# Kernel tuning notes

Hardware: AMD Instinct MI355X
Metric: run time of the kernel (lower is better)

## Reference

```python
import jax, jax.numpy as jnp
import numpy as np

N = 50000      # nodes
E = 800000     # edges (avg degree 16)
H = 128        # hidden_dim
F_IN = 128     # node_in_dim
EPS = 1e-8     # torch cosine_similarity eps
ALPHA = 0.3


def _xavier(k, shape):
    fan_out, fan_in = shape
    lim = float(np.sqrt(6.0 / (fan_in + fan_out)))
    return jax.random.uniform(k, shape, minval=-lim, maxval=lim, dtype=jnp.float32)


PARAM_SHAPES = [
    ("w_lq", (H, 1)), ("w_lf", (H, F_IN)),
    ("wq0", (H, 1)), ("wq1", (H, H)), ("wq2", (H, H)),
    ("wx0", (H, F_IN)), ("wx1", (H, H)), ("wx2", (H, H)),
    ("wf0", (H, H)), ("wf1", (H, H)), ("wf2", (H, H)),
    ("m1_w1", (H, H)), ("m1_w2", (H, H)),
    ("m2_w1", (1, H)), ("m2_w2", (1, 1)),
]
BIAS_OF = {"w_lq": "b_lq", "w_lf": "b_lf", "wq0": "bq0", "wq1": "bq1", "wq2": "bq2",
           "wx0": "bx0", "wx1": "bx1", "wx2": "bx2", "wf0": "bf0", "wf1": "bf1",
           "wf2": "bf2", "m1_w1": "m1_b1", "m1_w2": "m1_b2", "m2_w1": "m2_b1", "m2_w2": "m2_b2"}


def setup_inputs() -> dict:
    key = jax.random.key(0)
    ks = jax.random.split(key, 3 + len(PARAM_SHAPES))
    inp = {
        "q": 42,
        "feats": jax.random.normal(ks[0], (N, F_IN), dtype=jnp.float32),
        "edge_index": jax.random.randint(ks[1], (2, E), 0, N, dtype=jnp.int64),
        "neg_edge_index": jax.random.randint(ks[2], (2, E), 0, N, dtype=jnp.int64),
    }
    for i, (name, shape) in enumerate(PARAM_SHAPES):
        inp[name] = _xavier(ks[3 + i], shape)
        inp[BIAS_OF[name]] = jnp.zeros((shape[0],), jnp.float32)
    return inp


def _forward(q, feats, edge_index, neg_edge_index,
             w_lq, b_lq, w_lf, b_lf,
             wq0, bq0, wq1, bq1, wq2, bq2,
             wx0, bx0, wx1, bx1, wx2, bx2,
             wf0, bf0, wf1, bf1, wf2, bf2,
             m1_w1, m1_b1, m1_w2, m1_b2,
             m2_w1, m2_b1, m2_w2, m2_b2):
    n = feats.shape[0]
    src, dst = edge_index[0], edge_index[1]

    # GCN symmetric normalization with self-loops (edge_weight = 1)
    deg = jax.ops.segment_sum(jnp.ones(src.shape[0], feats.dtype), dst, num_segments=n) + 1.0
    dis = deg ** -0.5
    norm_e = dis[src] * dis[dst]        # per-edge norm
    inv_deg = 1.0 / deg                 # self-loop norm d^-1/2 * d^-1/2

    def lin(x, W, b):
        return x @ W.T + b

    def gcn(x, W, b):
        xw = x @ W.T                                                      # [n,H]
        agg = jax.ops.segment_sum(xw[src] * norm_e[:, None], dst, num_segments=n)
        return agg + xw * inv_deg[:, None] + b

    querys = jnp.zeros((n, 1), feats.dtype).at[q, 0].set(1.0)
    querys_ = lin(querys, w_lq, b_lq)
    feats_ = lin(feats, w_lf, b_lf)

    # layer 0
    hq = jax.nn.relu(gcn(querys, wq0, bq0))
    h = jax.nn.relu(gcn(feats, wx0, bx0))
    hf = jax.nn.relu(hq + h + gcn(querys_ + feats_, wf0, bf0))
    # middle layer (num_layers - 2 == 1 iteration, eval mode: dropout identity)
    hq = jax.nn.relu(gcn(hq, wq1, bq1))
    h = jax.nn.relu(gcn(h, wx1, bx1))
    hf = jax.nn.relu(hq + h + gcn(hf, wf1, bf1))
    # final layer (no relu)
    hq = gcn(hq, wq2, bq2)
    h = gcn(h, wx2, bx2)
    hf = hq + h + gcn(hf, wf2, bf2)

    x = lin(jax.nn.relu(lin(hf, m1_w1, m1_b1)), m1_w2, m1_b2)  # mlp1

    # ---- decode (attack_type != 'proposed') ----
    q_emb = x[q]
    qn = jnp.maximum(jnp.linalg.norm(q_emb), EPS)

    def cos_q(v):  # cosine similarity of rows of v with q_emb (torch eps semantics)
        vn = jnp.maximum(jnp.linalg.norm(v, axis=-1), EPS)
        return (v @ q_emb) / (vn * qn)

    # reconstruct loss: BCE-with-logits on cosine edge scores
    pos_s = cos_q((x[src] + x[dst]) * 0.5)
    neg_s = cos_q((x[neg_edge_index[0]] + x[neg_edge_index[1]]) * 0.5)
    loss_recon = jnp.mean(jax.nn.softplus(-pos_s)) + jnp.mean(jax.nn.softplus(neg_s))

    sim_xq = cos_q(x)                                            # [n]
    sim_xx = lin(jax.nn.relu(lin(x, m2_w1, m2_b1)), m2_w2, m2_b2)[:, 0]  # mlp2
    sim = ((1.0 - ALPHA) * sim_xq + ALPHA * sim_xx) * 2.0
    return jax.nn.sigmoid(sim), loss_recon


def reference(q, feats, edge_index, neg_edge_index,
              w_lq, b_lq, w_lf, b_lf,
              wq0, bq0, wq1, bq1, wq2, bq2,
              wx0, bx0, wx1, bx1, wx2, bx2,
              wf0, bf0, wf1, bf1, wf2, bf2,
              m1_w1, m1_b1, m1_w2, m1_b2,
              m2_w1, m2_b1, m2_w2, m2_b2):
    return _forward(q, feats, edge_index, neg_edge_index,
                    w_lq, b_lq, w_lf, b_lf,
                    wq0, bq0, wq1, bq1, wq2, bq2,
                    wx0, bx0, wx1, bx1, wx2, bx2,
                    wf0, bf0, wf1, bf1, wf2, bf2,
                    m1_w1, m1_b1, m1_w2, m1_b2,
                    m2_w1, m2_b1, m2_w2, m2_b2)
```

## Files before the change

### kernel.cpp

```cpp
#include <hip/hip_runtime.h>
#include <math.h>

#define N_NODES 50000
#define N_EDGES 800000
#define EPSV 1e-8f
#define ALPHA 0.3f

typedef __attribute__((ext_vector_type(8))) unsigned short ushort8;
typedef __attribute__((ext_vector_type(4))) float floatx4;
typedef __attribute__((ext_vector_type(2))) long longx2;
typedef _Float16 half8 __attribute__((ext_vector_type(8)));
typedef _Float16 half2v __attribute__((ext_vector_type(2)));

__device__ inline unsigned short f2h(float f) {
    union { _Float16 h; unsigned short u; } c; c.h = (_Float16)f; return c.u;
}
__device__ inline float h2f(unsigned short u) {
    union { unsigned short u; _Float16 h; } c; c.u = u; return (float)c.h;
}
__device__ inline unsigned char f2e4m3(float f) {
    unsigned u = __float_as_uint(f);
    unsigned s = (u >> 24) & 0x80u;
    float af = fabsf(f);
    if (af >= 464.f) return (unsigned char)(s | 0x7Eu);
    if (af < 0.015625f) {
        int m = (int)rintf(af * 512.f);
        return (unsigned char)(s | (unsigned)m);
    }
    unsigned au = __float_as_uint(af);
    unsigned mant = au & 0x7FFFFFu;
    unsigned lsb = (mant >> 20) & 1u;
    mant += 0x7FFFFu + lsb;
    unsigned exp32 = (au >> 23) + (mant >> 23);
    mant &= 0x7FFFFFu;
    unsigned e8 = exp32 - 127u + 7u;
    return (unsigned char)(s | (e8 << 3) | (mant >> 20));
}


__global__ __launch_bounds__(256) void k_count(const int* __restrict__ ei,
                                               int* __restrict__ cnt) {
    int e = blockIdx.x * 256 + threadIdx.x;
    if (e < N_EDGES) atomicAdd(&cnt[ei[N_EDGES + e]], 1);
}

__global__ __launch_bounds__(256) void k_invdis(const int* __restrict__ cnt,
                                                float* __restrict__ dis,
                                                float* __restrict__ inv) {
    int i = blockIdx.x * 256 + threadIdx.x;
    if (i < N_NODES) {
        float d = (float)cnt[i] + 1.0f;
        dis[i] = 1.0f / sqrtf(d);
        inv[i] = 1.0f / d;
    }
}

__global__ __launch_bounds__(256) void k_scan_partial(const int* __restrict__ cnt,
                                                      int* __restrict__ partial) {
    int b = blockIdx.x, t = threadIdx.x;
    int base = b * 1024 + t * 4;
    int s = 0;
#pragma unroll
    for (int j = 0; j < 4; ++j) {
        int idx = base + j;
        if (idx < N_NODES) s += cnt[idx];
    }
// ... 38 lines not shown
    for (int off = 1; off < 256; off <<= 1) {
        int v = 0;
        if (t >= off) v = sh[t - off];
        __syncthreads();
        sh[t] += v;
        __syncthreads();
    }
    int texcl = sh[t] - s;
    int pre = partial[b] + texcl;
#pragma unroll
    for (int j = 0; j < 4; ++j) {
        int idx = base + j;
        if (idx < N_NODES) rowptr[idx] = pre;
        pre += c[j];
    }
}

__global__ __launch_bounds__(256) void k_fill(const int* __restrict__ ei,
                                              const int* __restrict__ rowptr,
                                              int* __restrict__ cursor,
                                              int* __restrict__ col) {
    int e = blockIdx.x * 256 + threadIdx.x;
    if (e < N_EDGES) {
        int d = ei[N_EDGES + e];
        int pos = rowptr[d] + atomicAdd(&cursor[d], 1);
        col[pos] = ei[e];
    }
}

__global__ __launch_bounds__(256) void k_t(const int* __restrict__ ei,
                                           const int* __restrict__ qp,
                                           const float* __restrict__ dis,
                                           const float* __restrict__ inv,
                                           float* __restrict__ t) {
    int e = blockIdx.x * 256 + threadIdx.x;
    int q = *qp;
    if (e == 0) atomicAdd(&t[q], inv[q]);
    if (e < N_EDGES && ei[e] == q) {
        int d = ei[N_EDGES + e];
        atomicAdd(&t[d], dis[q] * dis[d]);
    }
}

__global__ void k_flag(const float* __restrict__ bq0, const float* __restrict__ bq1,
                       int* __restrict__ flag) {
    int j = threadIdx.x;
    float v = (j < 128) ? bq0[j] : bq1[j - 128];
    unsigned long long b = __ballot(v != 0.f);
    __shared__ int bad[4];
    if ((j & 63) == 0) bad[j >> 6] = (b != 0ull);
    __syncthreads();
    if (j == 0) flag[0] = !(bad[0] | bad[1] | bad[2] | bad[3]);
}

__global__ void k_r0(const int* __restrict__ gflag, const float* __restrict__ wq0,
                     float* __restrict__ r0) {
    if (*gflag != 1) return;
    int j = threadIdx.x;
    r0[j] = fmaxf(wq0[j], 0.f);
}

template <int RELU>
__global__ void k_matvec(const int* __restrict__ gflag, const float* __restrict__ W,
                         const float* __restrict__ vin, float* __restrict__ vout) {
    if (*gflag != 1) return;
    int c = blockIdx.x, l = threadIdx.x;
    float2 w = *(const float2*)(W + c * 128 + 2 * l);
    float2 v = *(const float2*)(vin + 2 * l);
    float s = w.x * v.x + w.y * v.y;
#pragma unroll
    for (int m = 1; m < 64; m <<= 1) s += __shfl_xor(s, m, 64);
    if (l == 0) vout[c] = RELU ? fmaxf(s, 0.f) : s;
}

__global__ __launch_bounds__(256) void k_spmv(const int* __restrict__ gflag,
                                              const int* __restrict__ rowptr,
                                              const int* __restrict__ col,
                                              const float* __restrict__ dis,
                                              const float* __restrict__ inv,
                                              const float* __restrict__ vin,
                                              float* __restrict__ vout) {
    if (*gflag != 1) return;
    int i = blockIdx.x * 256 + threadIdx.x;
    if (i >= N_NODES) return;
    int r0 = rowptr[i], r1 = rowptr[i + 1];
    float s = 0.f;
    for (int e = r0; e < r1; ++e) {
        int c = col[e];
        s += dis[c] * vin[c];
    }
    vout[i] = fmaf(inv[i], vin[i], dis[i] * s);
}

__global__ __launch_bounds__(256) void k_cast(const float* __restrict__ in,
                                              unsigned short* __restrict__ out, int n8) {
    int id = blockIdx.x * 256 + threadIdx.x;
    if (id >= n8) return;
    const float4 a = *(const float4*)(in + id * 8);
    const float4 b = *(const float4*)(in + id * 8 + 4);
    ushort8 o;
    o[0] = f2h(a.x); o[1] = f2h(a.y); o[2] = f2h(a.z); o[3] = f2h(a.w);
    o[4] = f2h(b.x); o[5] = f2h(b.y); o[6] = f2h(b.z); o[7] = f2h(b.w);
    *(ushort8*)(out + id * 8) = o;
}

struct WPack { const float* w[11]; };
__global__ __launch_bounds__(256) void k_castw(WPack wp, unsigned short* __restrict__ out) {
    int m = blockIdx.y;
    int id = blockIdx.x * 256 + threadIdx.x;
    const float* src = wp.w[m] + id * 8;
    float4 a = *(const float4*)src;
    float4 b = *(const float4*)(src + 4);
    ushort8 o;
    o[0] = f2h(a.x); o[1] = f2h(a.y); o[2] = f2h(a.z); o[3] = f2h(a.w);
    o[4] = f2h(b.x); o[5] = f2h(b.y); o[6] = f2h(b.z); o[7] = f2h(b.w);
    *(ushort8*)(out + m * 16384 + id * 8) = o;
}

__global__ __launch_bounds__(256) void k_cast8(const float* __restrict__ xf,
                                               unsigned char* __restrict__ xq8) {
    int id = blockIdx.x * 256 + threadIdx.x;
    int node = id >> 3, c = id & 7;
    if (node >= N_NODES) return;
    int kb = c >> 1, mb = (c & 1) * 2;
    const float* base = xf + (size_t)node * 128;
    const float* p0 = base + mb * 32 + kb * 8;
    const float* p1 = base + (mb + 1) * 32 + kb * 8;
    union { unsigned char b[16]; uint4 u; } o;
#pragma unroll
    for (int j = 0; j < 8; ++j) o.b[j] = f2e4m3(p0[j]);
#pragma unroll
    for (int j = 0; j < 8; ++j) o.b[8 + j] = f2e4m3(p1[j]);
    *(uint4*)(xq8 + (size_t)node * 128 + c * 16) = o.u;
}


template <int RELU, int NADD, int HASB2, int WOUT, int RK1>
__global__ __launch_bounds__(256) void k_gemm(
    const unsigned short* __restrict__ A, int As,
    const unsigned short* __restrict__ Wb,
    const float* __restrict__ bias, const float* __restrict__ bias2,
    const unsigned short* __restrict__ add1, int a1s,
    const unsigned short* __restrict__ add2, int a2s,
    const float* __restrict__ u, const float* __restrict__ vq,
    const int* __restrict__ gflag, int want,
    unsigned short* __restrict__ outh, int ohs,
    float* __restrict__ outf, int ofs, int nrows) {
    if (gflag && *gflag != want) return;
    __shared__ unsigned short Al[128 * 128];
    __shared__ unsigned short Wl[128 * 128];
    const int tid = threadIdx.x;
    const int row0 = blockIdx.x * 128;
    const int wv = tid >> 6;
    const int t4 = tid >> 4, c16 = tid & 15;

#pragma unroll
    for (int it = 0; it < 8; ++it) {
        int r = it * 16 + t4;
        int gr = row0 + r; if (gr > nrows - 1) gr = nrows - 1;
        int sw = (c16 * 16) ^ ((r & 7) << 4);
        const char* srcA = (const char*)(A + (size_t)gr * As) + sw;
        __builtin_amdgcn_global_load_lds(
            (const __attribute__((address_space(1))) void*)srcA,
            (__attribute__((address_space(3))) void*)(Al + it * 2048 + wv * 512),
            16, 0, 0);
        const char* srcW = (const char*)(Wb + r * 128) + sw;
        __builtin_amdgcn_global_load_lds(
            (const __attribute__((address_space(1))) void*)srcW,
            (__attribute__((address_space(3))) void*)(Wl + it * 2048 + wv * 512),
            16, 0, 0);
    }
    __syncthreads();

    const int l = tid & 63;
    const int lr = l & 15, lg = l >> 4;
    const int sx = (lr & 7) << 4;

    floatx4 acc[8][2];
#pragma unroll
    for (int i = 0; i < 8; ++i)
#pragma unroll
        for (int j = 0; j < 2; ++j) acc[i][j] = (floatx4){0.f, 0.f, 0.f, 0.f};

#pragma unroll
    for (int ks = 0; ks < 4; ++ks) {
        int ko = (ks * 64 + lg * 16) ^ sx;
        half8 bfr[2];
#pragma unroll
        for (int ct = 0; ct < 2; ++ct) {
            int c = wv * 32 + ct * 16 + lr;
            bfr[ct] = *(const half8*)((char*)Wl + c * 256 + ko);
        }
#pragma unroll
        for (int rt = 0; rt < 8; ++rt) {
            int r = rt * 16 + lr;
            half8 af = *(const half8*)((char*)Al + r * 256 + ko);
            acc[rt][0] = __builtin_amdgcn_mfma_f32_16x16x32_f16(af, bfr[0], acc[rt][0], 0, 0, 0);
            acc[rt][1] = __builtin_amdgcn_mfma_f32_16x16x32_f16(af, bfr[1], acc[rt][1], 0, 0, 0);
        }
    }

#pragma unroll
    for (int ct = 0; ct < 2; ++ct) {
        int colc = wv * 32 + ct * 16 + lr;
        float bv = bias[colc];
        if (HASB2) bv += bias2[colc];
        float vqc = RK1 ? vq[colc] : 0.f;
#pragma unroll
        for (int rt = 0; rt < 8; ++rt) {
            int rbase = row0 + rt * 16 + lg * 4;
#pragma unroll
            for (int reg = 0; reg < 4; ++reg) {
                int r = rbase + reg;
                if (r >= nrows) continue;
                float v = acc[rt][ct][reg] + bv;
                if (RK1) v = fmaf(u[r], vqc, v);
                if (NADD >= 1) v += h2f(add1[(size_t)r * a1s + colc]);
                if (NADD >= 2) v += h2f(add2[(size_t)r * a2s + colc]);
                if (RELU) v = fmaxf(v, 0.f);
                if (WOUT) outf[(size_t)r * ofs + colc] = v;
                else outh[(size_t)r * ohs + colc] = f2h(v);
            }
        }
    }
}


template <int NUM>
__global__ __launch_bounds__(256) void k_agg(
    const int* __restrict__ gflag, int want,
    const int* __restrict__ rowptr, const int* __restrict__ col,
    const float* __restrict__ dis, const float* __restrict__ inv,
    const unsigned short* __restrict__ in0, int s0,
    const unsigned short* __restrict__ in1, int s1,
    const unsigned short* __restrict__ in2, int s2,
    unsigned short* __restrict__ out, int o0, int o1, int o2) {
    if (gflag && *gflag != want) return;
    int i = blockIdx.x * 4 + (threadIdx.x >> 6);
    int l = threadIdx.x & 63;
    int g = l >> 4, li = l & 15;
    int r0 = rowptr[i], r1 = rowptr[i + 1];

    half2v accA[NUM][4], accB[NUM][4];
#pragma unroll
    for (int b = 0; b < NUM; ++b)
#pragma unroll
        for (int j = 0; j < 4; ++j) {
            accA[b][j] = (half2v){(_Float16)0, (_Float16)0};
            accB[b][j] = (half2v){(_Float16)0, (_Float16)0};
        }

    union U8 { ushort8 u; half2v h[4]; };
    const unsigned short* ins[3] = {in0, in1, in2};
    const int ss[3] = {s0, s1, s2};

    for (int base = r0; base < r1; base += 8) {
        int eA = base + g, eB = base + 4 + g;
        int sA = i; float wA = 0.f;
        if (eA < r1) { sA = col[eA]; wA = dis[sA]; }
        int sB = i; float wB = 0.f;
// ... 23 lines not shown
            c.h = accA[b][j] + accB[b][j];
            o.i = __shfl_xor(c.i, 16, 64); c.h += o.h;
            o.i = __shfl_xor(c.i, 32, 64); c.h += o.h;
            accA[b][j] = c.h;
        }
    if (g == 0) {
        float di = dis[i], iv = inv[i];
        const int oo[3] = {o0, o1, o2};
#pragma unroll
        for (int b = 0; b < NUM; ++b) {
            U8 sv;
            sv.u = *(const ushort8*)(ins[b] + (size_t)i * ss[b] + li * 8);
            ushort8 o;
#pragma unroll
            for (int j = 0; j < 4; ++j) {
                float a0 = fmaf(di, (float)accA[b][j][0], iv * (float)sv.h[j][0]);
                float a1 = fmaf(di, (float)accA[b][j][1], iv * (float)sv.h[j][1]);
                o[2 * j] = f2h(a0);
                o[2 * j + 1] = f2h(a1);
            }
            *(ushort8*)(out + (size_t)i * 384 + oo[b] + li * 8) = o;
        }
    }
}

__global__ __launch_bounds__(256) void k_hq0(const int* __restrict__ gflag,
                                             const float* __restrict__ t,
                                             const float* __restrict__ wq0,
                                             const float* __restrict__ bq0,
                                             unsigned short* __restrict__ B1h) {
    if (*gflag != 0) return;
    int gidx = blockIdx.x * 256 + threadIdx.x;
    int i = gidx >> 7, j = gidx & 127;
    B1h[(size_t)i * 384 + j] = f2h(fmaxf(fmaf(t[i], wq0[j], bq0[j]), 0.f));
}

__global__ void k_addwlq(const int* __restrict__ qp, const float* __restrict__ w_lq,
                         unsigned short* __restrict__ z0h) {
    int j = threadIdx.x;
    int q = *qp;
    z0h[(size_t)q * 128 + j] = f2h(h2f(z0h[(size_t)q * 128 + j]) + w_lq[j]);
}


__global__ void k_qemb(const int* __restrict__ qp, const float* __restrict__ xf,
                       float* __restrict__ qe) {
// ... 41 lines not shown
        float s2 = fmaxf(l1, 0.f) * m2w2[0] + m2b2[0];
        float sim = ((1.f - ALPHA) * simq + ALPHA * s2) * 2.f;
        out[node] = 1.f / (1.f + expf(-sim));
        a[node] = dq;
        n2[node] = dx;
    }
}

__global__ __launch_bounds__(256) void k_loss(const int* __restrict__ ei,
                                              const int* __restrict__ nei,
                                              const unsigned char* __restrict__ xq8,
                                              const float* __restrict__ a,
                                              const float* __restrict__ n2,
                                              const float* __restrict__ qe,
                                              float* __restrict__ lossout) {
    int l = threadIdx.x & 63, wvi = threadIdx.x >> 6;
    int i16 = l & 15;
    int kb = l >> 4;
    int gw = blockIdx.x * 4 + wvi;
    const int NW = gridDim.x * 4;
    const int NT = 2 * N_EDGES / 16;
    float qn = qe[128];
    float local = 0.f;

    int t = gw;
    for (; t + NW < NT; t += 2 * NW) {
        int baseA = t * 16;
        int negA = baseA >= N_EDGES;
        const int* EpA = negA ? nei : ei;
        int eoA = negA ? baseA - N_EDGES : baseA;
        int sA = EpA[eoA + i16], dA = EpA[eoA + i16 + N_EDGES];

        int baseB = (t + NW) * 16;
        int negB = baseB >= N_EDGES;
        const int* EpB = negB ? nei : ei;
        int eoB = negB ? baseB - N_EDGES : baseB;
        int sB = EpB[eoB + i16], dB = EpB[eoB + i16 + N_EDGES];

        const unsigned char* psA = xq8 + (size_t)sA * 128 + kb * 32;
        const unsigned char* pdA = xq8 + (size_t)dA * 128 + kb * 32;
        longx2 a01A = *(const longx2*)psA;
        longx2 a23A = *(const longx2*)(psA + 16);
        longx2 b01A = *(const longx2*)pdA;
        longx2 b23A = *(const longx2*)(pdA + 16);

        const unsigned char* psB = xq8 + (size_t)sB * 128 + kb * 32;
        const unsigned char* pdB = xq8 + (size_t)dB * 128 + kb * 32;
        longx2 a01B = *(const longx2*)psB;
        longx2 a23B = *(const longx2*)(psB + 16);
        longx2 b01B = *(const longx2*)pdB;
        longx2 b23B = *(const longx2*)(pdB + 16);

        float n2sA = 0.f, n2dA = 0.f, asA = 0.f, adA = 0.f;
        float n2sB = 0.f, n2dB = 0.f, asB = 0.f, adB = 0.f;
        if (l < 16) {
            n2sA = n2[sA]; n2dA = n2[dA]; asA = a[sA]; adA = a[dA];
            n2sB = n2[sB]; n2dB = n2[dB]; asB = a[sB]; adB = a[dB];
        }

        int r = l & 3;
        int srcl = ((i16 >> 2) << 4) + i16;
        {
            floatx4 acc = (floatx4){0.f, 0.f, 0.f, 0.f};
            acc = __builtin_amdgcn_mfma_f32_16x16x32_fp8_fp8(a01A[0], b01A[0], acc, 0, 0, 0);
            acc = __builtin_amdgcn_mfma_f32_16x16x32_fp8_fp8(a01A[1], b01A[1], acc, 0, 0, 0);
            acc = __builtin_amdgcn_mfma_f32_16x16x32_fp8_fp8(a23A[0], b23A[0], acc, 0, 0, 0);
            acc = __builtin_amdgcn_mfma_f32_16x16x32_fp8_fp8(a23A[1], b23A[1], acc, 0, 0, 0);
            float v = acc[0];
            v = (r == 1) ? acc[1] : v;
            v = (r == 2) ? acc[2] : v;
            v = (r == 3) ? acc[3] : v;
            float dsd = __int_as_float(
                __builtin_amdgcn_ds_bpermute(srcl << 2, __float_as_int(v)));
            if (l < 16) {
                float nv = 0.25f * (n2sA + n2dA + 2.f * dsd);
                float vn = fmaxf(sqrtf(fmaxf(nv, 0.f)), EPSV);
                float cs = (0.5f * (asA + adA)) / (vn * qn);
                float sg = negA ? cs : -cs;
                local += log1pf(expf(sg));
            }
        }
        {
            floatx4 acc = (floatx4){0.f, 0.f, 0.f, 0.f};
            acc = __builtin_amdgcn_mfma_f32_16x16x32_fp8_fp8(a01B[0], b01B[0], acc, 0, 0, 0);
            acc = __builtin_amdgcn_mfma_f32_16x16x32_fp8_fp8(a01B[1], b01B[1], acc, 0, 0, 0);
            acc = __builtin_amdgcn_mfma_f32_16x16x32_fp8_fp8(a23B[0], b23B[0], acc, 0, 0, 0);
            acc = __builtin_amdgcn_mfma_f32_16x16x32_fp8_fp8(a23B[1], b23B[1], acc, 0, 0, 0);
            float v = acc[0];
            v = (r == 1) ? acc[1] : v;
            v = (r == 2) ? acc[2] : v;
            v = (r == 3) ? acc[3] : v;
            float dsd = __int_as_float(
                __builtin_amdgcn_ds_bpermute(srcl << 2, __float_as_int(v)));
            if (l < 16) {
                float nv = 0.25f * (n2sB + n2dB + 2.f * dsd);
                float vn = fmaxf(sqrtf(fmaxf(nv, 0.f)), EPSV);
                float cs = (0.5f * (asB + adB)) / (vn * qn);
                float sg = negB ? cs : -cs;
                local += log1pf(expf(sg));
            }
        }
    }
    if (t < NT) {
        int base = t * 16;
        int neg = base >= N_EDGES;
        const int* Ep = neg ? nei : ei;
        int eo = neg ? base - N_EDGES : base;
        int s = Ep[eo + i16], d = Ep[eo + i16 + N_EDGES];
        const unsigned char* ps = xq8 + (size_t)s * 128 + kb * 32;
        const unsigned char* pd = xq8 + (size_t)d * 128 + kb * 32;
        longx2 a01 = *(const longx2*)ps;
        longx2 a23 = *(const longx2*)(ps + 16);
        longx2 b01 = *(const longx2*)pd;
        longx2 b23 = *(const longx2*)(pd + 16);
        floatx4 acc = (floatx4){0.f, 0.f, 0.f, 0.f};
        acc = __builtin_amdgcn_mfma_f32_16x16x32_fp8_fp8(a01[0], b01[0], acc, 0, 0, 0);
        acc = __builtin_amdgcn_mfma_f32_16x16x32_fp8_fp8(a01[1], b01[1], acc, 0, 0, 0);
        acc = __builtin_amdgcn_mfma_f32_16x16x32_fp8_fp8(a23[0], b23[0], acc, 0, 0, 0);
        acc = __builtin_amdgcn_mfma_f32_16x16x32_fp8_fp8(a23[1], b23[1], acc, 0, 0, 0);
        int r = l & 3;
        float v = acc[0];
        v = (r == 1) ? acc[1] : v;
        v = (r == 2) ? acc[2] : v;
        v = (r == 3) ? acc[3] : v;
        int srcl = ((i16 >> 2) << 4) + i16;
        float dsd = __int_as_float(
            __builtin_amdgcn_ds_bpermute(srcl << 2, __float_as_int(v)));
        if (l < 16) {
            float nv = 0.25f * (n2[s] + n2[d] + 2.f * dsd);
            float vn = fmaxf(sqrtf(fmaxf(nv, 0.f)), EPSV);
            float cs = (0.5f * (a[s] + a[d])) / (vn * qn);
            float sg = neg ? cs : -cs;
            local += log1pf(expf(sg));
        }
    }
    local += __shfl_xor(local, 1, 64);
    local += __shfl_xor(local, 2, 64);
    local += __shfl_xor(local, 4, 64);
    local += __shfl_xor(local, 8, 64);
    __shared__ float sh[4];
    if (l == 0) sh[wvi] = local;
    __syncthreads();
    if (threadIdx.x == 0)
        atomicAdd(lossout, (sh[0] + sh[1] + sh[2] + sh[3]) * (1.f / N_EDGES));
}


extern "C" void kernel_launch(void* const* d_in, const int* in_sizes, int n_in,
// ... 48 lines not shown
    unsigned short* z0h = (unsigned short*)alloc((size_t)N_NODES * 128 * 2);
    unsigned short* B1h = (unsigned short*)alloc((size_t)N_NODES * 384 * 2);
    unsigned short* B2h = (unsigned short*)alloc((size_t)N_NODES * 384 * 2);
    unsigned char* xq8 = (unsigned char*)alloc((size_t)N_NODES * 128);
    float* xf = (float*)alloc((size_t)N_NODES * 128 * 4);

    const int EB = (N_EDGES + 255) / 256;
    const int NB = (N_NODES + 255) / 256;
    const int NP = (N_NODES + 1023) / 1024;
    const int GB = (N_NODES + 127) / 128;

    hipMemsetAsync(cnt, 0, N_NODES * 4, stream);
    hipMemsetAsync(cursor, 0, N_NODES * 4, stream);
    hipMemsetAsync(t, 0, N_NODES * 4, stream);
    hipMemsetAsync(out + N_NODES, 0, 4, stream);

    k_count<<<EB, 256, 0, stream>>>(ei, cnt);
    k_invdis<<<NB, 256, 0, stream>>>(cnt, dis, inv);
    k_scan_partial<<<NP, 256, 0, stream>>>(cnt, partial);
    k_scan_mid<<<1, 64, 0, stream>>>(partial, rowptr);
    k_scan_final<<<NP, 256, 0, stream>>>(cnt, partial, rowptr);
    k_fill<<<EB, 256, 0, stream>>>(ei, rowptr, cursor, col);
    k_t<<<EB, 256, 0, stream>>>(ei, qp, dis, inv, t);
    k_flag<<<1, 256, 0, stream>>>(bq0, bq1, flag);
    k_cast<<<(N_NODES * 128 / 8 + 255) / 256, 256, 0, stream>>>(feats, featsh,
                                                                N_NODES * 128 / 8);
    WPack wp{{w_lf, wx0, wf0, wq1, wx1, wf1, wq2, wx2, wf2, m1w1, m1w2}};
    k_castw<<<dim3(8, 11), 256, 0, stream>>>(wp, Wb);

    k_r0<<<1, 128, 0, stream>>>(flag, wq0, r0v);
    k_spmv<<<NB, 256, 0, stream>>>(flag, rowptr, col, dis, inv, t, u1);
    k_spmv<<<NB, 256, 0, stream>>>(flag, rowptr, col, dis, inv, u1, u2);
    k_matvec<1><<<128, 64, 0, stream>>>(flag, wq1, r0v, r1v);
    k_matvec<0><<<128, 64, 0, stream>>>(flag, wq2, r1v, g2v);

    k_gemm<0, 0, 1, 0, 0><<<GB, 256, 0, stream>>>(featsh, 128, Wb + 0 * 16384, b_lf, b_lq,
                                                  nullptr, 0, nullptr, 0,
                                                  nullptr, nullptr, nullptr, 0,
                                                  z0h, 128, nullptr, 0, N_NODES);
    k_addwlq<<<1, 128, 0, stream>>>(qp, w_lq, z0h);

    k_hq0<<<(N_NODES * 128) / 256, 256, 0, stream>>>(flag, t, wq0, bq0, B1h);
    k_agg<2><<<N_NODES / 4, 256, 0, stream>>>(nullptr, 0, rowptr, col, dis, inv,
                                              featsh, 128, z0h, 128, nullptr, 0,
                                              B2h, 128, 256, 0);
    k_gemm<1, 0, 0, 0, 0><<<GB, 256, 0, stream>>>(B2h + 128, 384, Wb + 1 * 16384, bx0, nullptr,
                                                  nullptr, 0, nullptr, 0,
                                                  nullptr, nullptr, nullptr, 0,
                                                  B1h + 128, 384, nullptr, 0, N_NODES);
    k_gemm<1, 2, 0, 0, 0><<<GB, 256, 0, stream>>>(B2h + 256, 384, Wb + 2 * 16384, bf0, nullptr,
                                                  B1h + 0, 384, B1h + 128, 384,
                                                  nullptr, nullptr, flag, 0,
                                                  B1h + 256, 384, nullptr, 0, N_NODES);
    k_gemm<1, 1, 0, 0, 1><<<GB, 256, 0, stream>>>(B2h + 256, 384, Wb + 2 * 16384, bf0, nullptr,
                                                  B1h + 128, 384, nullptr, 0,
                                                  t, r0v, flag, 1,
                                                  B1h + 256, 384, nullptr, 0, N_NODES);

    k_agg<3><<<N_NODES / 4, 256, 0, stream>>>(flag, 0, rowptr, col, dis, inv,
                                              B1h, 384, B1h + 128, 384, B1h + 256, 384,
                                              B2h, 0, 128, 256);
    k_agg<2><<<N_NODES / 4, 256, 0, stream>>>(flag, 1, rowptr, col, dis, inv,
                                              B1h + 128, 384, B1h + 256, 384, nullptr, 0,
                                              B2h, 128, 256, 0);
    k_gemm<1, 0, 0, 0, 0><<<GB, 256, 0, stream>>>(B2h + 0, 384, Wb + 3 * 16384, bq1, nullptr,
                                                  nullptr, 0, nullptr, 0,
                                                  nullptr, nullptr, flag, 0,
                                                  B1h + 0, 384, nullptr, 0, N_NODES);
    k_gemm<1, 0, 0, 0, 0><<<GB, 256, 0, stream>>>(B2h + 128, 384, Wb + 4 * 16384, bx1, nullptr,
                                                  nullptr, 0, nullptr, 0,
                                                  nullptr, nullptr, nullptr, 0,
                                                  B1h + 128, 384, nullptr, 0, N_NODES);
    k_gemm<1, 2, 0, 0, 0><<<GB, 256, 0, stream>>>(B2h + 256, 384, Wb + 5 * 16384, bf1, nullptr,
                                                  B1h + 0, 384, B1h + 128, 384,
                                                  nullptr, nullptr, flag, 0,
                                                  B1h + 256, 384, nullptr, 0, N_NODES);
    k_gemm<1, 1, 0, 0, 1><<<GB, 256, 0, stream>>>(B2h + 256, 384, Wb + 5 * 16384, bf1, nullptr,
                                                  B1h + 128, 384, nullptr, 0,
                                                  u1, r1v, flag, 1,
                                                  B1h + 256, 384, nullptr, 0, N_NODES);

    k_agg<3><<<N_NODES / 4, 256, 0, stream>>>(flag, 0, rowptr, col, dis, inv,
                                              B1h, 384, B1h + 128, 384, B1h + 256, 384,
                                              B2h, 0, 128, 256);
    k_agg<2><<<N_NODES / 4, 256, 0, stream>>>(flag, 1, rowptr, col, dis, inv,
                                              B1h + 128, 384, B1h + 256, 384, nullptr, 0,
                                              B2h, 128, 256, 0);
    k_gemm<0, 0, 0, 0, 0><<<GB, 256, 0, stream>>>(B2h + 0, 384, Wb + 6 * 16384, bq2, nullptr,
                                                  nullptr, 0, nullptr, 0,
                                                  nullptr, nullptr, flag, 0,
                                                  B1h + 0, 384, nullptr, 0, N_NODES);
    k_gemm<0, 0, 0, 0, 0><<<GB, 256, 0, stream>>>(B2h + 128, 384, Wb + 7 * 16384, bx2, nullptr,
                                                  nullptr, 0, nullptr, 0,
                                                  nullptr, nullptr, nullptr, 0,
                                                  B1h + 128, 384, nullptr, 0, N_NODES);
    k_gemm<0, 2, 0, 0, 0><<<GB, 256, 0, stream>>>(B2h + 256, 384, Wb + 8 * 16384, bf2, nullptr,
                                                  B1h + 0, 384, B1h + 128, 384,
                                                  nullptr, nullptr, flag, 0,
                                                  B1h + 256, 384, nullptr, 0, N_NODES);
    k_gemm<0, 1, 1, 0, 1><<<GB, 256, 0, stream>>>(B2h + 256, 384, Wb + 8 * 16384, bf2, bq2,
                                                  B1h + 128, 384, nullptr, 0,
                                                  u2, g2v, flag, 1,
                                                  B1h + 256, 384, nullptr, 0, N_NODES);

    k_gemm<1, 0, 0, 0, 0><<<GB, 256, 0, stream>>>(B1h + 256, 384, Wb + 9 * 16384, m1b1, nullptr,
                                                  nullptr, 0, nullptr, 0,
                                                  nullptr, nullptr, nullptr, 0,
                                                  B2h + 0, 384, nullptr, 0, N_NODES);
    k_gemm<0, 0, 0, 1, 0><<<GB, 256, 0, stream>>>(B2h + 0, 384, Wb + 10 * 16384, m1b2, nullptr,
                                                  nullptr, 0, nullptr, 0,
                                                  nullptr, nullptr, nullptr, 0,
                                                  nullptr, 0, xf, 128, N_NODES);

    k_cast8<<<(N_NODES * 8 + 255) / 256, 256, 0, stream>>>(xf, xq8);
    k_qemb<<<1, 128, 0, stream>>>(qp, xf, qe);
    k_node<<<N_NODES / 4, 256, 0, stream>>>(xf, qe, m2w1, m2b1, m2w2, m2b2, out, a, n2);
    k_loss<<<2048, 256, 0, stream>>>(ei, nei, xq8, a, n2, qe, out + N_NODES);
}
```

Before: 612.2 us.

## Merge flag-gated kernel pairs, fuse fp8 cast into final GEMM, deepen loss pipelining

Several kernels that were launched in pairs and early-exited on a runtime flag are merged into single kernels that branch on the flag inside: aggregation, the fused-layer GEMM, and the rank-1 setup matvecs. The fp8 quantisation of the output embedding now happens in the last GEMM's epilogue, which removes the separate cast kernel and one re-read of the fp32 output. The loss kernel now keeps four edge batches in flight instead of two, and edge-index loads use nontemporal hints. Together these are meant to cut launch count and redundant memory traffic, at the cost of more registers in the loss loop and scattered byte stores in the GEMM epilogue.

```diff
diff --git a/kernel.cpp b/kernel.cpp
--- a/kernel.cpp
+++ b/kernel.cpp
@@ -36,12 +36,15 @@
     unsigned e8 = exp32 - 127u + 7u;
     return (unsigned char)(s | (e8 << 3) | (mant >> 20));
 }
+__device__ inline int qperm(int k) {
+    return ((k >> 3) & 3) * 32 + (k >> 5) * 8 + (k & 7);
+}
 
 
 __global__ __launch_bounds__(256) void k_count(const int* __restrict__ ei,
                                                int* __restrict__ cnt) {
     int e = blockIdx.x * 256 + threadIdx.x;
-    if (e < N_EDGES) atomicAdd(&cnt[ei[N_EDGES + e]], 1);
+    if (e < N_EDGES) atomicAdd(&cnt[__builtin_nontemporal_load(ei + N_EDGES + e)], 1);
 }
 
 __global__ __launch_bounds__(256) void k_invdis(const int* __restrict__ cnt,
@@ -126,9 +129,9 @@
                                               int* __restrict__ col) {
     int e = blockIdx.x * 256 + threadIdx.x;
     if (e < N_EDGES) {
-        int d = ei[N_EDGES + e];
+        int d = __builtin_nontemporal_load(ei + N_EDGES + e);
         int pos = rowptr[d] + atomicAdd(&cursor[d], 1);
-        col[pos] = ei[e];
+        col[pos] = __builtin_nontemporal_load(ei + e);
     }
 }
 
@@ -140,41 +143,45 @@
     int e = blockIdx.x * 256 + threadIdx.x;
     int q = *qp;
     if (e == 0) atomicAdd(&t[q], inv[q]);
-    if (e < N_EDGES && ei[e] == q) {
+    if (e < N_EDGES && __builtin_nontemporal_load(ei + e) == q) {
         int d = ei[N_EDGES + e];
         atomicAdd(&t[d], dis[q] * dis[d]);
     }
 }
 
-__global__ void k_flag(const float* __restrict__ bq0, const float* __restrict__ bq1,
-                       int* __restrict__ flag) {
+__global__ void k_rank1(const float* __restrict__ bq0, const float* __restrict__ bq1,
+                        const float* __restrict__ wq0, const float* __restrict__ wq1,
+                        const float* __restrict__ wq2, int* __restrict__ flag,
+                        float* __restrict__ r0v, float* __restrict__ r1v,
+                        float* __restrict__ g2v) {
     int j = threadIdx.x;
-    float v = (j < 128) ? bq0[j] : bq1[j - 128];
-    unsigned long long b = __ballot(v != 0.f);
-    __shared__ int bad[4];
+    unsigned long long b = __ballot(bq0[j] != 0.f || bq1[j] != 0.f);
+    __shared__ int bad[2];
+    __shared__ float r0s[128], r1s[128];
     if ((j & 63) == 0) bad[j >> 6] = (b != 0ull);
     __syncthreads();
-    if (j == 0) flag[0] = !(bad[0] | bad[1] | bad[2] | bad[3]);
-}
-
-__global__ void k_r0(const int* __restrict__ gflag, const float* __restrict__ wq0,
-                     float* __restrict__ r0) {
-    if (*gflag != 1) return;
-    int j = threadIdx.x;
-    r0[j] = fmaxf(wq0[j], 0.f);
-}
-
-template <int RELU>
-__global__ void k_matvec(const int* __restrict__ gflag, const float* __restrict__ W,
-                         const float* __restrict__ vin, float* __restrict__ vout) {
-    if (*gflag != 1) return;
-    int c = blockIdx.x, l = threadIdx.x;
-    float2 w = *(const float2*)(W + c * 128 + 2 * l);
-    float2 v = *(const float2*)(vin + 2 * l);
-    float s = w.x * v.x + w.y * v.y;
-#pragma unroll
-    for (int m = 1; m < 64; m <<= 1) s += __shfl_xor(s, m, 64);
-    if (l == 0) vout[c] = RELU ? fmaxf(s, 0.f) : s;
+    int fl = !(bad[0] | bad[1]);
+    if (j == 0) flag[0] = fl;
+    if (!fl) return;
+    float r0 = fmaxf(wq0[j], 0.f);
+    r0s[j] = r0;
+    r0v[j] = r0;
+    __syncthreads();
+    float s = 0.f;
+    for (int k = 0; k < 128; k += 4) {
+        float4 w = *(const float4*)(wq1 + j * 128 + k);
+        s += w.x * r0s[k] + w.y * r0s[k + 1] + w.z * r0s[k + 2] + w.w * r0s[k + 3];
+    }
+    float r1 = fmaxf(s, 0.f);
+    r1s[j] = r1;
+    r1v[j] = r1;
+    __syncthreads();
+    float s2 = 0.f;
+    for (int k = 0; k < 128; k += 4) {
+        float4 w = *(const float4*)(wq2 + j * 128 + k);
+        s2 += w.x * r1s[k] + w.y * r1s[k + 1] + w.z * r1s[k + 2] + w.w * r1s[k + 3];
+    }
+    g2v[j] = s2;
 }
 
 __global__ __launch_bounds__(256) void k_spmv(const int* __restrict__ gflag,
@@ -221,40 +228,12 @@
     *(ushort8*)(out + m * 16384 + id * 8) = o;
 }
 
-__global__ __launch_bounds__(256) void k_cast8(const float* __restrict__ xf,
-                                               unsigned char* __restrict__ xq8) {
-    int id = blockIdx.x * 256 + threadIdx.x;
-    int node = id >> 3, c = id & 7;
-    if (node >= N_NODES) return;
-    int kb = c >> 1, mb = (c & 1) * 2;
-    const float* base = xf + (size_t)node * 128;
-    const float* p0 = base + mb * 32 + kb * 8;
-    const float* p1 = base + (mb + 1) * 32 + kb * 8;
-    union { unsigned char b[16]; uint4 u; } o;
-#pragma unroll
-    for (int j = 0; j < 8; ++j) o.b[j] = f2e4m3(p0[j]);
-#pragma unroll
-    for (int j = 0; j < 8; ++j) o.b[8 + j] = f2e4m3(p1[j]);
-    *(uint4*)(xq8 + (size_t)node * 128 + c * 16) = o.u;
-}
-
-
-template <int RELU, int NADD, int HASB2, int WOUT, int RK1>
-__global__ __launch_bounds__(256) void k_gemm(
+
+__device__ __forceinline__ void gemm_core(
     const unsigned short* __restrict__ A, int As,
-    const unsigned short* __restrict__ Wb,
-    const float* __restrict__ bias, const float* __restrict__ bias2,
-    const unsigned short* __restrict__ add1, int a1s,
-    const unsigned short* __restrict__ add2, int a2s,
-    const float* __restrict__ u, const float* __restrict__ vq,
-    const int* __restrict__ gflag, int want,
-    unsigned short* __restrict__ outh, int ohs,
-    float* __restrict__ outf, int ofs, int nrows) {
-    if (gflag && *gflag != want) return;
-    __shared__ unsigned short Al[128 * 128];
-    __shared__ unsigned short Wl[128 * 128];
+    const unsigned short* __restrict__ Wb, int nrows, int row0,
+    unsigned short* Al, unsigned short* Wl, floatx4 (&acc)[8][2]) {
     const int tid = threadIdx.x;
-    const int row0 = blockIdx.x * 128;
     const int wv = tid >> 6;
     const int t4 = tid >> 4, c16 = tid & 15;
 
@@ -280,7 +259,6 @@
     const int lr = l & 15, lg = l >> 4;
     const int sx = (lr & 7) << 4;
 
-    floatx4 acc[8][2];
 #pragma unroll
     for (int i = 0; i < 8; ++i)
 #pragma unroll
@@ -303,13 +281,31 @@
             acc[rt][1] = __builtin_amdgcn_mfma_f32_16x16x32_f16(af, bfr[1], acc[rt][1], 0, 0, 0);
         }
     }
-
+}
+
+template <int RELU, int HASB2, int WOUT>
+__global__ __launch_bounds__(256) void k_gemm(
+    const unsigned short* __restrict__ A, int As,
+    const unsigned short* __restrict__ Wb,
+    const float* __restrict__ bias, const float* __restrict__ bias2,
+    const int* __restrict__ gflag, int want,
+    unsigned short* __restrict__ outh, int ohs,
+    float* __restrict__ outf, unsigned char* __restrict__ outq, int nrows) {
+    if (gflag && *gflag != want) return;
+    __shared__ unsigned short Al[128 * 128];
+    __shared__ unsigned short Wl[128 * 128];
+    const int row0 = blockIdx.x * 128;
+    floatx4 acc[8][2];
+    gemm_core(A, As, Wb, nrows, row0, Al, Wl, acc);
+
+    const int l = threadIdx.x & 63, wv = threadIdx.x >> 6;
+    const int lr = l & 15, lg = l >> 4;
 #pragma unroll
     for (int ct = 0; ct < 2; ++ct) {
         int colc = wv * 32 + ct * 16 + lr;
         float bv = bias[colc];
         if (HASB2) bv += bias2[colc];
-        float vqc = RK1 ? vq[colc] : 0.f;
+        int qp_ = WOUT == 2 ? qperm(colc) : 0;
 #pragma unroll
         for (int rt = 0; rt < 8; ++rt) {
             int rbase = row0 + rt * 16 + lg * 4;
@@ -318,28 +314,73 @@
                 int r = rbase + reg;
                 if (r >= nrows) continue;
                 float v = acc[rt][ct][reg] + bv;
-                if (RK1) v = fmaf(u[r], vqc, v);
-                if (NADD >= 1) v += h2f(add1[(size_t)r * a1s + colc]);
-                if (NADD >= 2) v += h2f(add2[(size_t)r * a2s + colc]);
                 if (RELU) v = fmaxf(v, 0.f);
-                if (WOUT) outf[(size_t)r * ofs + colc] = v;
-                else outh[(size_t)r * ohs + colc] = f2h(v);
+                if (WOUT == 2) {
+                    outf[(size_t)r * 128 + colc] = v;
+                    outq[(size_t)r * 128 + qp_] = f2e4m3(v);
+                } else {
+                    outh[(size_t)r * ohs + colc] = f2h(v);
+                }
             }
         }
     }
 }
 
+template <int RELU>
+__global__ __launch_bounds__(256) void k_gemmF(
+    const unsigned short* __restrict__ A, int As,
+    const unsigned short* __restrict__ Wb,
+    const float* __restrict__ bias, const float* __restrict__ bias2,
+    const unsigned short* __restrict__ addh, int ahs,
+    const unsigned short* __restrict__ addhq, int aqs,
+    const float* __restrict__ u, const float* __restrict__ vq,
+    const int* __restrict__ gflag,
+    unsigned short* __restrict__ outh, int ohs, int nrows) {
+    __shared__ unsigned short Al[128 * 128];
+    __shared__ unsigned short Wl[128 * 128];
+    const int row0 = blockIdx.x * 128;
+    floatx4 acc[8][2];
+    gemm_core(A, As, Wb, nrows, row0, Al, Wl, acc);
+
+    const int fl = *gflag;
+    const int l = threadIdx.x & 63, wv = threadIdx.x >> 6;
+    const int lr = l & 15, lg = l >> 4;
+#pragma unroll
+    for (int ct = 0; ct < 2; ++ct) {
+        int colc = wv * 32 + ct * 16 + lr;
+        float bv = bias[colc];
+        float vqc = 0.f;
+        if (fl) {
+            vqc = vq[colc];
+            if (bias2) bv += bias2[colc];
+        }
+#pragma unroll
+        for (int rt = 0; rt < 8; ++rt) {
+            int rbase = row0 + rt * 16 + lg * 4;
+#pragma unroll
+            for (int reg = 0; reg < 4; ++reg) {
+                int r = rbase + reg;
+                if (r >= nrows) continue;
+                float v = acc[rt][ct][reg] + bv;
+                if (fl) v = fmaf(u[r], vqc, v);
+                else v += h2f(addhq[(size_t)r * aqs + colc]);
+                v += h2f(addh[(size_t)r * ahs + colc]);
+                if (RELU) v = fmaxf(v, 0.f);
+                outh[(size_t)r * ohs + colc] = f2h(v);
+            }
+        }
+    }
+}
+
 
 template <int NUM>
-__global__ __launch_bounds__(256) void k_agg(
-    const int* __restrict__ gflag, int want,
+__device__ __forceinline__ void agg_body(
     const int* __restrict__ rowptr, const int* __restrict__ col,
     const float* __restrict__ dis, const float* __restrict__ inv,
     const unsigned short* __restrict__ in0, int s0,
     const unsigned short* __restrict__ in1, int s1,
     const unsigned short* __restrict__ in2, int s2,
     unsigned short* __restrict__ out, int o0, int o1, int o2) {
-    if (gflag && *gflag != want) return;
     int i = blockIdx.x * 4 + (threadIdx.x >> 6);
     int l = threadIdx.x & 63;
     int g = l >> 4, li = l & 15;
@@ -409,6 +450,28 @@
             *(ushort8*)(out + (size_t)i * 384 + oo[b] + li * 8) = o;
         }
     }
+}
+
+__global__ __launch_bounds__(256) void k_agg0(
+    const int* __restrict__ rowptr, const int* __restrict__ col,
+    const float* __restrict__ dis, const float* __restrict__ inv,
+    const unsigned short* __restrict__ featsh, const unsigned short* __restrict__ z0h,
+    unsigned short* __restrict__ out) {
+    agg_body<2>(rowptr, col, dis, inv, featsh, 128, z0h, 128, nullptr, 0,
+                out, 128, 256, 0);
+}
+
+__global__ __launch_bounds__(256) void k_aggL(
+    const int* __restrict__ gflag,
+    const int* __restrict__ rowptr, const int* __restrict__ col,
+    const float* __restrict__ dis, const float* __restrict__ inv,
+    const unsigned short* __restrict__ B1h, unsigned short* __restrict__ B2h) {
+    if (*gflag == 1)
+        agg_body<2>(rowptr, col, dis, inv, B1h + 128, 384, B1h + 256, 384,
+                    nullptr, 0, B2h, 128, 256, 0);
+    else
+        agg_body<3>(rowptr, col, dis, inv, B1h, 384, B1h + 128, 384,
+                    B1h + 256, 384, B2h, 0, 128, 256);
 }
 
 __global__ __launch_bounds__(256) void k_hq0(const int* __restrict__ gflag,
@@ -496,86 +559,60 @@
     const int NT = 2 * N_EDGES / 16;
     float qn = qe[128];
     float local = 0.f;
+    const int rsel = l & 3;
+    const int srcl = ((i16 >> 2) << 4) + i16;
 
     int t = gw;
-    for (; t + NW < NT; t += 2 * NW) {
-        int baseA = t * 16;
-        int negA = baseA >= N_EDGES;
-        const int* EpA = negA ? nei : ei;
-        int eoA = negA ? baseA - N_EDGES : baseA;
-        int sA = EpA[eoA + i16], dA = EpA[eoA + i16 + N_EDGES];
-
-        int baseB = (t + NW) * 16;
-        int negB = baseB >= N_EDGES;
-        const int* EpB = negB ? nei : ei;
-        int eoB = negB ? baseB - N_EDGES : baseB;
-        int sB = EpB[eoB + i16], dB = EpB[eoB + i16 + N_EDGES];
-
-        const unsigned char* psA = xq8 + (size_t)sA * 128 + kb * 32;
-        const unsigned char* pdA = xq8 + (size_t)dA * 128 + kb * 32;
-        longx2 a01A = *(const longx2*)psA;
-        longx2 a23A = *(const longx2*)(psA + 16);
-        longx2 b01A = *(const longx2*)pdA;
-        longx2 b23A = *(const longx2*)(pdA + 16);
-
-        const unsigned char* psB = xq8 + (size_t)sB * 128 + kb * 32;
-        const unsigned char* pdB = xq8 + (size_t)dB * 128 + kb * 32;
-        longx2 a01B = *(const longx2*)psB;
-        longx2 a23B = *(const longx2*)(psB + 16);
-        longx2 b01B = *(const longx2*)pdB;
-        longx2 b23B = *(const longx2*)(pdB + 16);
-
-        float n2sA = 0.f, n2dA = 0.f, asA = 0.f, adA = 0.f;
-        float n2sB = 0.f, n2dB = 0.f, asB = 0.f, adB = 0.f;
-        if (l < 16) {
-            n2sA = n2[sA]; n2dA = n2[dA]; asA = a[sA]; adA = a[dA];
-            n2sB = n2[sB]; n2dB = n2[dB]; asB = a[sB]; adB = a[dB];
-        }
-
-        int r = l & 3;
-        int srcl = ((i16 >> 2) << 4) + i16;
-        {
+    for (; t + 3 * NW < NT; t += 4 * NW) {
+        int s[4], d[4], neg[4];
+        longx2 a01[4], a23[4], b01[4], b23[4];
+        float n2s[4], n2d[4], as_[4], ad_[4];
+#pragma unroll
+        for (int p_ = 0; p_ < 4; ++p_) {
+            int base = (t + p_ * NW) * 16;
+            neg[p_] = base >= N_EDGES;
+            const int* Ep = neg[p_] ? nei : ei;
+            int eo = neg[p_] ? base - N_EDGES : base;
+            s[p_] = __builtin_nontemporal_load(Ep + eo + i16);
+            d[p_] = __builtin_nontemporal_load(Ep + eo + i16 + N_EDGES);
+        }
+#pragma unroll
+        for (int p_ = 0; p_ < 4; ++p_) {
+            const unsigned char* ps = xq8 + (size_t)s[p_] * 128 + kb * 32;
+            const unsigned char* pd = xq8 + (size_t)d[p_] * 128 + kb * 32;
+            a01[p_] = *(const longx2*)ps;
+            a23[p_] = *(const longx2*)(ps + 16);
+            b01[p_] = *(const longx2*)pd;
+            b23[p_] = *(const longx2*)(pd + 16);
+            n2s[p_] = 0.f; n2d[p_] = 0.f; as_[p_] = 0.f; ad_[p_] = 0.f;
+            if (l < 16) {
+                n2s[p_] = n2[s[p_]]; n2d[p_] = n2[d[p_]];
+                as_[p_] = a[s[p_]]; ad_[p_] = a[d[p_]];
+            }
+        }
+#pragma unroll
+        for (int p_ = 0; p_ < 4; ++p_) {
             floatx4 acc = (floatx4){0.f, 0.f, 0.f, 0.f};
-            acc = __builtin_amdgcn_mfma_f32_16x16x32_fp8_fp8(a01A[0], b01A[0], acc, 0, 0, 0);
-            acc = __builtin_amdgcn_mfma_f32_16x16x32_fp8_fp8(a01A[1], b01A[1], acc, 0, 0, 0);
-            acc = __builtin_amdgcn_mfma_f32_16x16x32_fp8_fp8(a23A[0], b23A[0], acc, 0, 0, 0);
-            acc = __builtin_amdgcn_mfma_f32_16x16x32_fp8_fp8(a23A[1], b23A[1], acc, 0, 0, 0);
+            acc = __builtin_amdgcn_mfma_f32_16x16x32_fp8_fp8(a01[p_][0], b01[p_][0], acc, 0, 0, 0);
+            acc = __builtin_amdgcn_mfma_f32_16x16x32_fp8_fp8(a01[p_][1], b01[p_][1], acc, 0, 0, 0);
+            acc = __builtin_amdgcn_mfma_f32_16x16x32_fp8_fp8(a23[p_][0], b23[p_][0], acc, 0, 0, 0);
+            acc = __builtin_amdgcn_mfma_f32_16x16x32_fp8_fp8(a23[p_][1], b23[p_][1], acc, 0, 0, 0);
             float v = acc[0];
-            v = (r == 1) ? acc[1] : v;
-            v = (r == 2) ? acc[2] : v;
-            v = (r == 3) ? acc[3] : v;
+            v = (rsel == 1) ? acc[1] : v;
+            v = (rsel == 2) ? acc[2] : v;
+            v = (rsel == 3) ? acc[3] : v;
             float dsd = __int_as_float(
                 __builtin_amdgcn_ds_bpermute(srcl << 2, __float_as_int(v)));
             if (l < 16) {
-                float nv = 0.25f * (n2sA + n2dA + 2.f * dsd);
+                float nv = 0.25f * (n2s[p_] + n2d[p_] + 2.f * dsd);
                 float vn = fmaxf(sqrtf(fmaxf(nv, 0.f)), EPSV);
-                float cs = (0.5f * (asA + adA)) / (vn * qn);
-                float sg = negA ? cs : -cs;
+                float cs = (0.5f * (as_[p_] + ad_[p_])) / (vn * qn);
+                float sg = neg[p_] ? cs : -cs;
                 local += log1pf(expf(sg));
             }
         }
-        {
-            floatx4 acc = (floatx4){0.f, 0.f, 0.f, 0.f};
-            acc = __builtin_amdgcn_mfma_f32_16x16x32_fp8_fp8(a01B[0], b01B[0], acc, 0, 0, 0);
-            acc = __builtin_amdgcn_mfma_f32_16x16x32_fp8_fp8(a01B[1], b01B[1], acc, 0, 0, 0);
-            acc = __builtin_amdgcn_mfma_f32_16x16x32_fp8_fp8(a23B[0], b23B[0], acc, 0, 0, 0);
-            acc = __builtin_amdgcn_mfma_f32_16x16x32_fp8_fp8(a23B[1], b23B[1], acc, 0, 0, 0);
-            float v = acc[0];
-            v = (r == 1) ? acc[1] : v;
-            v = (r == 2) ? acc[2] : v;
-            v = (r == 3) ? acc[3] : v;
-            float dsd = __int_as_float(
-                __builtin_amdgcn_ds_bpermute(srcl << 2, __float_as_int(v)));
-            if (l < 16) {
-                float nv = 0.25f * (n2sB + n2dB + 2.f * dsd);
-                float vn = fmaxf(sqrtf(fmaxf(nv, 0.f)), EPSV);
-                float cs = (0.5f * (asB + adB)) / (vn * qn);
-                float sg = negB ? cs : -cs;
-                local += log1pf(expf(sg));
-            }
-        }
-    }
-    if (t < NT) {
+    }
+    for (; t < NT; t += NW) {
         int base = t * 16;
         int neg = base >= N_EDGES;
         const int* Ep = neg ? nei : ei;
@@ -592,12 +629,10 @@
         acc = __builtin_amdgcn_mfma_f32_16x16x32_fp8_fp8(a01[1], b01[1], acc, 0, 0, 0);
         acc = __builtin_amdgcn_mfma_f32_16x16x32_fp8_fp8(a23[0], b23[0], acc, 0, 0, 0);
         acc = __builtin_amdgcn_mfma_f32_16x16x32_fp8_fp8(a23[1], b23[1], acc, 0, 0, 0);
-        int r = l & 3;
         float v = acc[0];
-        v = (r == 1) ? acc[1] : v;
-        v = (r == 2) ? acc[2] : v;
-        v = (r == 3) ? acc[3] : v;
-        int srcl = ((i16 >> 2) << 4) + i16;
+        v = (rsel == 1) ? acc[1] : v;
+        v = (rsel == 2) ? acc[2] : v;
+        v = (rsel == 3) ? acc[3] : v;
         float dsd = __int_as_float(
             __builtin_amdgcn_ds_bpermute(srcl << 2, __float_as_int(v)));
         if (l < 16) {
@@ -692,97 +727,49 @@
     k_scan_final<<<NP, 256, 0, stream>>>(cnt, partial, rowptr);
     k_fill<<<EB, 256, 0, stream>>>(ei, rowptr, cursor, col);
     k_t<<<EB, 256, 0, stream>>>(ei, qp, dis, inv, t);
-    k_flag<<<1, 256, 0, stream>>>(bq0, bq1, flag);
+    k_rank1<<<1, 128, 0, stream>>>(bq0, bq1, wq0, wq1, wq2, flag, r0v, r1v, g2v);
     k_cast<<<(N_NODES * 128 / 8 + 255) / 256, 256, 0, stream>>>(feats, featsh,
                                                                 N_NODES * 128 / 8);
     WPack wp{{w_lf, wx0, wf0, wq1, wx1, wf1, wq2, wx2, wf2, m1w1, m1w2}};
     k_castw<<<dim3(8, 11), 256, 0, stream>>>(wp, Wb);
-
-    k_r0<<<1, 128, 0, stream>>>(flag, wq0, r0v);
     k_spmv<<<NB, 256, 0, stream>>>(flag, rowptr, col, dis, inv, t, u1);
     k_spmv<<<NB, 256, 0, stream>>>(flag, rowptr, col, dis, inv, u1, u2);
-    k_matvec<1><<<128, 64, 0, stream>>>(flag, wq1, r0v, r1v);
-    k_matvec<0><<<128, 64, 0, stream>>>(flag, wq2, r1v, g2v);
-
-    k_gemm<0, 0, 1, 0, 0><<<GB, 256, 0, stream>>>(featsh, 128, Wb + 0 * 16384, b_lf, b_lq,
-                                                  nullptr, 0, nullptr, 0,
-                                                  nullptr, nullptr, nullptr, 0,
-                                                  z0h, 128, nullptr, 0, N_NODES);
+
+    k_gemm<0, 1, 0><<<GB, 256, 0, stream>>>(featsh, 128, Wb + 0 * 16384, b_lf, b_lq,
+                                            nullptr, 0, z0h, 128, nullptr, nullptr, N_NODES);
     k_addwlq<<<1, 128, 0, stream>>>(qp, w_lq, z0h);
 
     k_hq0<<<(N_NODES * 128) / 256, 256, 0, stream>>>(flag, t, wq0, bq0, B1h);
-    k_agg<2><<<N_NODES / 4, 256, 0, stream>>>(nullptr, 0, rowptr, col, dis, inv,
-                                              featsh, 128, z0h, 128, nullptr, 0,
-                                              B2h, 128, 256, 0);
-    k_gemm<1, 0, 0, 0, 0><<<GB, 256, 0, stream>>>(B2h + 128, 384, Wb + 1 * 16384, bx0, nullptr,
-                                                  nullptr, 0, nullptr, 0,
-                                                  nullptr, nullptr, nullptr, 0,
-                                                  B1h + 128, 384, nullptr, 0, N_NODES);
-    k_gemm<1, 2, 0, 0, 0><<<GB, 256, 0, stream>>>(B2h + 256, 384, Wb + 2 * 16384, bf0, nullptr,
-                                                  B1h + 0, 384, B1h + 128, 384,
-                                                  nullptr, nullptr, flag, 0,
-                                                  B1h + 256, 384, nullptr, 0, N_NODES);
-    k_gemm<1, 1, 0, 0, 1><<<GB, 256, 0, stream>>>(B2h + 256, 384, Wb + 2 * 16384, bf0, nullptr,
-                                                  B1h + 128, 384, nullptr, 0,
-                                                  t, r0v, flag, 1,
-                                                  B1h + 256, 384, nullptr, 0, N_NODES);
-
-    k_agg<3><<<N_NODES / 4, 256, 0, stream>>>(flag, 0, rowptr, col, dis, inv,
-                                              B1h, 384, B1h + 128, 384, B1h + 256, 384,
-                                              B2h, 0, 128, 256);
-    k_agg<2><<<N_NODES / 4, 256, 0, stream>>>(flag, 1, rowptr, col, dis, inv,
-                                              B1h + 128, 384, B1h + 256, 384, nullptr, 0,
-                                              B2h, 128, 256, 0);
-    k_gemm<1, 0, 0, 0, 0><<<GB, 256, 0, stream>>>(B2h + 0, 384, Wb + 3 * 16384, bq1, nullptr,
-                                                  nullptr, 0, nullptr, 0,
-                                                  nullptr, nullptr, flag, 0,
-                                                  B1h + 0, 384, nullptr, 0, N_NODES);
-    k_gemm<1, 0, 0, 0, 0><<<GB, 256, 0, stream>>>(B2h + 128, 384, Wb + 4 * 16384, bx1, nullptr,
-                                                  nullptr, 0, nullptr, 0,
-                                                  nullptr, nullptr, nullptr, 0,
-                                                  B1h + 128, 384, nullptr, 0, N_NODES);
-    k_gemm<1, 2, 0, 0, 0><<<GB, 256, 0, stream>>>(B2h + 256, 384, Wb + 5 * 16384, bf1, nullptr,
-                                                  B1h + 0, 384, B1h + 128, 384,
-                                                  nullptr, nullptr, flag, 0,
-                                                  B1h + 256, 384, nullptr, 0, N_NODES);
-    k_gemm<1, 1, 0, 0, 1><<<GB, 256, 0, stream>>>(B2h + 256, 384, Wb + 5 * 16384, bf1, nullptr,
-                                                  B1h + 128, 384, nullptr, 0,
-                                                  u1, r1v, flag, 1,
-                                                  B1h + 256, 384, nullptr, 0, N_NODES);
-
-    k_agg<3><<<N_NODES / 4, 256, 0, stream>>>(flag, 0, rowptr, col, dis, inv,
-                                              B1h, 384, B1h + 128, 384, B1h + 256, 384,
-                                              B2h, 0, 128, 256);
-    k_agg<2><<<N_NODES / 4, 256, 0, stream>>>(flag, 1, rowptr, col, dis, inv,
-                                              B1h + 128, 384, B1h + 256, 384, nullptr, 0,
-                                              B2h, 128, 256, 0);
-    k_gemm<0, 0, 0, 0, 0><<<GB, 256, 0, stream>>>(B2h + 0, 384, Wb + 6 * 16384, bq2, nullptr,
-                                                  nullptr, 0, nullptr, 0,
-                                                  nullptr, nullptr, flag, 0,
-                                                  B1h + 0, 384, nullptr, 0, N_NODES);
-    k_gemm<0, 0, 0, 0, 0><<<GB, 256, 0, stream>>>(B2h + 128, 384, Wb + 7 * 16384, bx2, nullptr,
-                                                  nullptr, 0, nullptr, 0,
-                                                  nullptr, nullptr, nullptr, 0,
-                                                  B1h + 128, 384, nullptr, 0, N_NODES);
-    k_gemm<0, 2, 0, 0, 0><<<GB, 256, 0, stream>>>(B2h + 256, 384, Wb + 8 * 16384, bf2, nullptr,
-                                                  B1h + 0, 384, B1h + 128, 384,
-                                                  nullptr, nullptr, flag, 0,
-                                                  B1h + 256, 384, nullptr, 0, N_NODES);
-    k_gemm<0, 1, 1, 0, 1><<<GB, 256, 0, stream>>>(B2h + 256, 384, Wb + 8 * 16384, bf2, bq2,
-                                                  B1h + 128, 384, nullptr, 0,
-                                                  u2, g2v, flag, 1,
-                                                  B1h + 256, 384, nullptr, 0, N_NODES);
-
-    k_gemm<1, 0, 0, 0, 0><<<GB, 256, 0, stream>>>(B1h + 256, 384, Wb + 9 * 16384, m1b1, nullptr,
-                                                  nullptr, 0, nullptr, 0,
-                                                  nullptr, nullptr, nullptr, 0,
-                                                  B2h + 0, 384, nullptr, 0, N_NODES);
-    k_gemm<0, 0, 0, 1, 0><<<GB, 256, 0, stream>>>(B2h + 0, 384, Wb + 10 * 16384, m1b2, nullptr,
-                                                  nullptr, 0, nullptr, 0,
-                                                  nullptr, nullptr, nullptr, 0,
-                                                  nullptr, 0, xf, 128, N_NODES);
-
-    k_cast8<<<(N_NODES * 8 + 255) / 256, 256, 0, stream>>>(xf, xq8);
+    k_agg0<<<N_NODES / 4, 256, 0, stream>>>(rowptr, col, dis, inv, featsh, z0h, B2h);
+    k_gemm<1, 0, 0><<<GB, 256, 0, stream>>>(B2h + 128, 384, Wb + 1 * 16384, bx0, nullptr,
+                                            nullptr, 0, B1h + 128, 384, nullptr, nullptr, N_NODES);
+    k_gemmF<1><<<GB, 256, 0, stream>>>(B2h + 256, 384, Wb + 2 * 16384, bf0, nullptr,
+                                       B1h + 128, 384, B1h + 0, 384,
+                                       t, r0v, flag, B1h + 256, 384, N_NODES);
+
+    k_aggL<<<N_NODES / 4, 256, 0, stream>>>(flag, rowptr, col, dis, inv, B1h, B2h);
+    k_gemm<1, 0, 0><<<GB, 256, 0, stream>>>(B2h + 0, 384, Wb + 3 * 16384, bq1, nullptr,
+                                            flag, 0, B1h + 0, 384, nullptr, nullptr, N_NODES);
+    k_gemm<1, 0, 0><<<GB, 256, 0, stream>>>(B2h + 128, 384, Wb + 4 * 16384, bx1, nullptr,
+                                            nullptr, 0, B1h + 128, 384, nullptr, nullptr, N_NODES);
+    k_gemmF<1><<<GB, 256, 0, stream>>>(B2h + 256, 384, Wb + 5 * 16384, bf1, nullptr,
+                                       B1h + 128, 384, B1h + 0, 384,
+                                       u1, r1v, flag, B1h + 256, 384, N_NODES);
+
+    k_aggL<<<N_NODES / 4, 256, 0, stream>>>(flag, rowptr, col, dis, inv, B1h, B2h);
+    k_gemm<0, 0, 0><<<GB, 256, 0, stream>>>(B2h + 0, 384, Wb + 6 * 16384, bq2, nullptr,
+                                            flag, 0, B1h + 0, 384, nullptr, nullptr, N_NODES);
+    k_gemm<0, 0, 0><<<GB, 256, 0, stream>>>(B2h + 128, 384, Wb + 7 * 16384, bx2, nullptr,
+                                            nullptr, 0, B1h + 128, 384, nullptr, nullptr, N_NODES);
+    k_gemmF<0><<<GB, 256, 0, stream>>>(B2h + 256, 384, Wb + 8 * 16384, bf2, bq2,
+                                       B1h + 128, 384, B1h + 0, 384,
+                                       u2, g2v, flag, B1h + 256, 384, N_NODES);
+
+    k_gemm<1, 0, 0><<<GB, 256, 0, stream>>>(B1h + 256, 384, Wb + 9 * 16384, m1b1, nullptr,
+                                            nullptr, 0, B2h + 0, 384, nullptr, nullptr, N_NODES);
+    k_gemm<0, 0, 2><<<GB, 256, 0, stream>>>(B2h + 0, 384, Wb + 10 * 16384, m1b2, nullptr,
+                                            nullptr, 0, nullptr, 0, xf, xq8, N_NODES);
+
     k_qemb<<<1, 128, 0, stream>>>(qp, xf, qe);
     k_node<<<N_NODES / 4, 256, 0, stream>>>(xf, qe, m2w1, m2b1, m2w2, m2b2, out, a, n2);
     k_loss<<<2048, 256, 0, stream>>>(ei, nei, xq8, a, n2, qe, out + N_NODES);
```

After: 643.5 us. 1.05x slower.
